# Optimization experiments

Hardware: AMD Instinct MI355X
Metric: run time of the kernel (lower is better)

Reference implementation:

```python
import jax, jax.numpy as jnp
import numpy as np

N_NODES = 50000
N_EDGES = 800000
IN_FEAT = 1000
HID = 128
HEADS = 2
NEG_SLOPE = 0.2  # PyG GATConv default
EPS = 1e-16      # PyG softmax denom eps


def setup_inputs() -> dict:
    key = jax.random.key(0)
    ks = jax.random.split(key, 12)
    x = jax.random.normal(ks[0], (N_NODES, IN_FEAT), dtype=jnp.float32)
    edge_index = jax.random.randint(ks[1], (2, N_EDGES), 0, N_NODES, dtype=jnp.int64)
    readout_idx = jax.random.randint(ks[2], (1024,), 0, N_NODES, dtype=jnp.int64)
    s = 0.05
    return {
        "x": x,
        "edge_index": edge_index,
        "readout_idx": readout_idx,
        "W1": jax.random.normal(ks[3], (IN_FEAT, HEADS * HID), dtype=jnp.float32) * s,
        "att_src1": jax.random.normal(ks[4], (HEADS, HID), dtype=jnp.float32) * s,
        "att_dst1": jax.random.normal(ks[5], (HEADS, HID), dtype=jnp.float32) * s,
        "b1": jax.random.normal(ks[6], (HEADS * HID,), dtype=jnp.float32) * s,
        "W2": jax.random.normal(ks[7], (HEADS * HID, 1), dtype=jnp.float32) * s,
        "att_src2": jax.random.normal(ks[8], (1, 1), dtype=jnp.float32) * s,
        "att_dst2": jax.random.normal(ks[9], (1, 1), dtype=jnp.float32) * s,
        "b2": jax.random.normal(ks[10], (1,), dtype=jnp.float32) * s,
    }


def gat_conv(x, edge_index, W, att_src, att_dst, bias, heads, out_dim, concat):
    """PyG GATConv with add_self_loops=False. x: [N, F_in]."""
    n = x.shape[0]
    src, dst = edge_index[0], edge_index[1]
    h = (x @ W).reshape(n, heads, out_dim)            # [N, H, D]
    a_src = jnp.einsum("nhd,hd->nh", h, att_src)      # [N, H]
    a_dst = jnp.einsum("nhd,hd->nh", h, att_dst)
    e = jax.nn.leaky_relu(a_src[src] + a_dst[dst], NEG_SLOPE)  # [E, H]
    # softmax over incoming edges of each destination node
    e_max = jax.ops.segment_max(e, dst, num_segments=n)
    e_exp = jnp.exp(e - e_max[dst])
    denom = jax.ops.segment_sum(e_exp, dst, num_segments=n)
    alpha = e_exp / (denom[dst] + EPS)                # [E, H]
    msg = h[src] * alpha[:, :, None]                  # [E, H, D]
    out = jax.ops.segment_sum(msg, dst, num_segments=n)  # [N, H, D]
    out = out.reshape(n, heads * out_dim) if concat else out.mean(axis=1)
    return out + bias


def reference(x, edge_index, readout_idx, W1, att_src1, att_dst1, b1,
              W2, att_src2, att_dst2, b2):
    # dropout is identity in eval mode
    h = gat_conv(x, edge_index, W1, att_src1, att_dst1, b1, HEADS, HID, True)
    h = jax.nn.relu(h)
    out = gat_conv(h, edge_index, W2, att_src2, att_dst2, b2, 1, 1, False)  # [N, 1]
    return out[readout_idx]  # [1024, 1]
```

## Files before the change

### kernel.cpp

```cpp
#include <hip/hip_runtime.h>
#include <hip/hip_bf16.h>
#include <math.h>

#define N_NODES 50000
#define N_EDGES 800000
#define IN_FEAT 1000
#define HID 128
#define HEADS 2
#define FOUT 256
#define NEG_SLOPE 0.2f
#define EPS 1e-16f

#define KPAD 1024
#define GEMM_NWG 782

typedef __bf16 bf16x8 __attribute__((ext_vector_type(8)));
typedef float f32x4 __attribute__((ext_vector_type(4)));

__device__ __forceinline__ float lrelu(float v) { return v > 0.f ? v : NEG_SLOPE * v; }

__device__ __forceinline__ ushort bf16rn(float v) {
  union { float f; unsigned u; } a; a.f = v;
  unsigned r = a.u + 0x7FFFu + ((a.u >> 16) & 1u);
  return (ushort)(r >> 16);
}
__device__ __forceinline__ void bf16split(float v, ushort& h, ushort& l) {
  h = bf16rn(v);
  union { float f; unsigned u; } b; b.u = ((unsigned)h) << 16;
  l = bf16rn(v - b.f);
}

__device__ __forceinline__ void gload_lds16(const void* g, void* l) {
  __builtin_amdgcn_global_load_lds((const __attribute__((address_space(1))) void*)g,
                                   (__attribute__((address_space(3))) void*)l, 16, 0, 0);
}

__global__ void hist_kernel(const int* __restrict__ dst, int* __restrict__ counts) {
  int e = blockIdx.x * blockDim.x + threadIdx.x;
  if (e < N_EDGES) atomicAdd(&counts[dst[e]], 1);
}

__global__ __launch_bounds__(1024) void scan1_kernel(const int* __restrict__ counts,
                                                     int* __restrict__ iscan,
                                                     int* __restrict__ bsum) {
  __shared__ int buf[1024];
  const int t = threadIdx.x;
  const int i = blockIdx.x * 1024 + t;
  int v = (i < N_NODES) ? counts[i] : 0;
  buf[t] = v;
  __syncthreads();
#pragma unroll
  for (int off = 1; off < 1024; off <<= 1) {
    int x = (t >= off) ? buf[t - off] : 0;
    __syncthreads();
    buf[t] += x;
    __syncthreads();
  }
  if (i < N_NODES) iscan[i] = buf[t];
  if (t == 1023) bsum[blockIdx.x] = buf[1023];
}

__global__ __launch_bounds__(64) void scan2_kernel(const int* __restrict__ bsum,
                                                   int* __restrict__ boff,
                                                   int* __restrict__ row_start, int nblk) {
  const int t = threadIdx.x;
  int v = (t < nblk) ? bsum[t] : 0;
  int s = v;
#pragma unroll
  for (int off = 1; off < 64; off <<= 1) {
    int y = __shfl_up(s, off, 64);
    if (t >= off) s += y;
  }
  if (t < nblk) boff[t] = s - v;
  if (t == nblk - 1) row_start[N_NODES] = s;
}

__global__ void scan3_kernel(const int* __restrict__ iscan, const int* __restrict__ counts,
                             const int* __restrict__ boff, int* __restrict__ row_start,
                             int* __restrict__ cursor) {
  int i = blockIdx.x * blockDim.x + threadIdx.x;
  if (i < N_NODES) {
    int rs = boff[i >> 10] + iscan[i] - counts[i];
    row_start[i] = rs;
    cursor[i] = rs;
  }
}

__global__ void scatter_kernel(const int* __restrict__ src, const int* __restrict__ dst,
                               int* __restrict__ cursor, int* __restrict__ csr_src) {
  int e = blockIdx.x * blockDim.x + threadIdx.x;
  if (e < N_EDGES) {
    int pos = atomicAdd(&cursor[dst[e]], 1);
    csr_src[pos] = src[e];
  }
}

__global__ __launch_bounds__(256) void cvtB_kernel(const float* __restrict__ B,
                                                   ushort* __restrict__ thi,
                                                   ushort* __restrict__ tlo) {
  int i = blockIdx.x * 256 + threadIdx.x;
  int nn = i >> 8;
  int k4 = (i & 255) << 2;
  ushort4 h, l;
#pragma unroll
  for (int j = 0; j < 4; ++j) {
    int k = k4 + j;
    float v = (k < IN_FEAT) ? B[(size_t)k * FOUT + nn] : 0.f;
    ushort hh, ll;
    bf16split(v, hh, ll);
    ((ushort*)&h)[j] = hh;
    ((ushort*)&l)[j] = ll;
  }
  *(ushort4*)(thi + (size_t)nn * KPAD + k4) = h;
  *(ushort4*)(tlo + (size_t)nn * KPAD + k4) = l;
}

__global__ __launch_bounds__(256, 2) void gemm_fused_kernel(
    const float* __restrict__ X,
    const ushort* __restrict__ Bhi, const ushort* __restrict__ Blo,
    float* __restrict__ C) {
  __shared__ ushort lAhi[128 * 64];
  __shared__ ushort lAlo[128 * 64];
  __shared__ ushort lBhi[128 * 64];
  __shared__ ushort lBlo[128 * 64];

  const int orig = blockIdx.x;
  const int q = GEMM_NWG >> 3, r = GEMM_NWG & 7;
  const int xcd = orig & 7, idx = orig >> 3;
  const int lin = (xcd < r) ? xcd * (q + 1) + idx : r * (q + 1) + (xcd - r) * q + idx;
  const int brow = (lin >> 1) * 128;
  const int bcol = (lin & 1) * 128;

  const int t = threadIdx.x;
  const int lane = t & 63, wid = t >> 6;
  const int wr = wid >> 1, wc = wid & 1;
  const int fr = lane & 15, g = lane >> 4;

  float4 areg[8];

  auto loadA = [&](int ks) {
#pragma unroll
    for (int i = 0; i < 4; ++i) {
      const int c = i * 256 + t;
      const int row = c >> 3, kc8 = c & 7;
      const int ksrc = kc8 ^ (row & 7);
      const int rowg = brow + row;
      const int kb = ks * 64 + ksrc * 8;
      if (rowg < N_NODES && kb < IN_FEAT) {
        const float* p = X + (size_t)rowg * IN_FEAT + kb;
        areg[2 * i] = *(const float4*)p;
        areg[2 * i + 1] = *(const float4*)(p + 4);
      } else {
        areg[2 * i] = make_float4(0.f, 0.f, 0.f, 0.f);
        areg[2 * i + 1] = make_float4(0.f, 0.f, 0.f, 0.f);
      }
    }
  };

  auto stageB = [&](int ks) {
    const int k0b = ks * 128;
#pragma unroll
    for (int i = 0; i < 4; ++i) {
      int u = i * 256 + t;
      int row = u >> 3;
      int inner = (u & 7) * 16;
      int soff = inner ^ ((row & 7) << 4);
      size_t boff = (size_t)(bcol + row) * (KPAD * 2) + k0b + soff;
      int loff = u * 16;
      gload_lds16((const char*)Bhi + boff, (char*)lBhi + loff);
      gload_lds16((const char*)Blo + boff, (char*)lBlo + loff);
    }
  };

  f32x4 acc[4][4];
  const f32x4 z4 = {0.f, 0.f, 0.f, 0.f};
#pragma unroll
  for (int m = 0; m < 4; ++m)
#pragma unroll
    for (int n = 0; n < 4; ++n) acc[m][n] = z4;

  loadA(0);
  const int NK = KPAD / 64;
  for (int ks = 0; ks < NK; ++ks) {
    union U8 { uint4 q; ushort us[8]; };
    U8 hiv[4], lov[4];
#pragma unroll
    for (int i = 0; i < 4; ++i) {
      const float* vv = (const float*)&areg[2 * i];
#pragma unroll
      for (int j = 0; j < 8; ++j) {
        unsigned u = __float_as_uint(vv[j]);
        ushort h = (ushort)(u >> 16);
        float hf = __uint_as_float(u & 0xFFFF0000u);
        float d = vv[j] - hf;
        ushort l = (ushort)(__float_as_uint(d) >> 16);
        hiv[i].us[j] = h;
        lov[i].us[j] = l;
      }
    }
    __syncthreads();
#pragma unroll
    for (int i = 0; i < 4; ++i) {
      const int c = i * 256 + t;
      *(uint4*)((char*)lAhi + c * 16) = hiv[i].q;
      *(uint4*)((char*)lAlo + c * 16) = lov[i].q;
    }
    stageB(ks);
    __syncthreads();
    if (ks + 1 < NK) loadA(ks + 1);
#pragma unroll
    for (int h = 0; h < 2; ++h) {
      bf16x8 ah[4], al[4], bh[4], bl[4];
#pragma unroll
      for (int m = 0; m < 4; ++m) {
        int row = wr * 64 + m * 16 + fr;
        int off = row * 128 + ((h * 64 + g * 16) ^ ((row & 7) << 4));
        ah[m] = *(const bf16x8*)((const char*)lAhi + off);
        al[m] = *(const bf16x8*)((const char*)lAlo + off);
      }
#pragma unroll
      for (int n = 0; n < 4; ++n) {
        int row = wc * 64 + n * 16 + fr;
        int off = row * 128 + ((h * 64 + g * 16) ^ ((row & 7) << 4));
        bh[n] = *(const bf16x8*)((const char*)lBhi + off);
        bl[n] = *(const bf16x8*)((const char*)lBlo + off);
      }
#pragma unroll
      for (int m = 0; m < 4; ++m)
#pragma unroll
        for (int n = 0; n < 4; ++n) {
          acc[m][n] = __builtin_amdgcn_mfma_f32_16x16x32_bf16(ah[m], bh[n], acc[m][n], 0, 0, 0);
          acc[m][n] = __builtin_amdgcn_mfma_f32_16x16x32_bf16(ah[m], bl[n], acc[m][n], 0, 0, 0);
          acc[m][n] = __builtin_amdgcn_mfma_f32_16x16x32_bf16(al[m], bh[n], acc[m][n], 0, 0, 0);
        }
    }
  }

#pragma unroll
  for (int m = 0; m < 4; ++m) {
    int growbase = brow + wr * 64 + m * 16 + g * 4;
#pragma unroll
    for (int n = 0; n < 4; ++n) {
      int gcol = bcol + wc * 64 + n * 16 + fr;
#pragma unroll
      for (int rr = 0; rr < 4; ++rr) {
        int grow = growbase + rr;
        if (grow < N_NODES) C[(size_t)grow * FOUT + gcol] = acc[m][n][rr];
      }
    }
  }
}

__global__ __launch_bounds__(64) void att1_kernel(const float* __restrict__ h1,
                                                  const float* __restrict__ as,
                                                  const float* __restrict__ ad,
                                                  float* __restrict__ asrc,
                                                  float* __restrict__ adst) {
  const int n = blockIdx.x;
  const int lane = threadIdx.x;
  const float* hr = h1 + (size_t)n * FOUT;
  float4 hv = *(const float4*)(hr + 4 * lane);
  float4 sv = *(const float4*)(as + 4 * lane);
  float4 dv = *(const float4*)(ad + 4 * lane);
  float ps = hv.x * sv.x + hv.y * sv.y + hv.z * sv.z + hv.w * sv.w;
  float pd = hv.x * dv.x + hv.y * dv.y + hv.z * dv.z + hv.w * dv.w;
#pragma unroll
  for (int off = 16; off > 0; off >>= 1) {
    ps += __shfl_xor(ps, off, 64);
    pd += __shfl_xor(pd, off, 64);
  }
  if ((lane & 31) == 0) {
    int hh = lane >> 5;
    asrc[2 * n + hh] = ps;
    adst[2 * n + hh] = pd;
  }
}

__global__ __launch_bounds__(64) void agg1_kernel(
    const float* __restrict__ h1, const float* __restrict__ asrc,
    const float* __restrict__ adst, const int* __restrict__ row_start,
    const int* __restrict__ csr_src, const float* __restrict__ b1,
    const float* __restrict__ W2, float* __restrict__ z) {
  const int n = blockIdx.x;
  const int lane = threadIdx.x;
  const bool head0 = lane < 32;
  const float ad0 = adst[2 * n], ad1 = adst[2 * n + 1];
  const int jb = row_start[n], je = row_start[n + 1];
  float ax = 0.f, ay = 0.f, az = 0.f, aw = 0.f;
  float m0 = -INFINITY, m1 = -INFINITY, s0 = 0.f, s1 = 0.f;

  for (int base = jb; base < je; base += 64) {
    int cnt = je - base;
    if (cnt > 64) cnt = 64;
    const bool act = lane < cnt;
    const int sr = csr_src[base + (act ? lane : 0)];
    float e0 = -INFINITY, e1 = -INFINITY;
    if (act) {
      e0 = lrelu(asrc[2 * sr] + ad0);
      e1 = lrelu(asrc[2 * sr + 1] + ad1);
    }
    float c0 = e0, c1 = e1;
#pragma unroll
    for (int off = 32; off > 0; off >>= 1) {
      c0 = fmaxf(c0, __shfl_xor(c0, off, 64));
      c1 = fmaxf(c1, __shfl_xor(c1, off, 64));
    }
    const float m0n = fmaxf(m0, c0), m1n = fmaxf(m1, c1);
    const float f0 = __expf(m0 - m0n), f1 = __expf(m1 - m1n);
    const float p0 = act ? __expf(e0 - m0n) : 0.f;
    const float p1 = act ? __expf(e1 - m1n) : 0.f;
    float t0 = p0, t1 = p1;
#pragma unroll
    for (int off = 32; off > 0; off >>= 1) {
      t0 += __shfl_xor(t0, off, 64);
      t1 += __shfl_xor(t1, off, 64);
    }
    s0 = s0 * f0 + t0;
    s1 = s1 * f1 + t1;
    m0 = m0n;
    m1 = m1n;
    const float f = head0 ? f0 : f1;
    ax *= f; ay *= f; az *= f; aw *= f;
    for (int j = 0; j < cnt; ++j) {
      const int srj = __shfl(sr, j, 64);
      const float pj0 = __shfl(p0, j, 64);
      const float pj1 = __shfl(p1, j, 64);
      const float pj = head0 ? pj0 : pj1;
      float4 hv = *(const float4*)(h1 + (size_t)srj * FOUT + 4 * lane);
      ax = fmaf(pj, hv.x, ax);
      ay = fmaf(pj, hv.y, ay);
      az = fmaf(pj, hv.z, az);
      aw = fmaf(pj, hv.w, aw);
    }
  }
  const float inv = head0 ? 1.f / (s0 + EPS) : 1.f / (s1 + EPS);
  float4 bv = *(const float4*)(b1 + 4 * lane);
  float4 wv = *(const float4*)(W2 + 4 * lane);
  float r0 = fmaxf(fmaf(ax, inv, bv.x), 0.f);
  float r1 = fmaxf(fmaf(ay, inv, bv.y), 0.f);
  float r2 = fmaxf(fmaf(az, inv, bv.z), 0.f);
  float r3 = fmaxf(fmaf(aw, inv, bv.w), 0.f);
  float part = r0 * wv.x + r1 * wv.y + r2 * wv.z + r3 * wv.w;
#pragma unroll
  for (int off = 32; off > 0; off >>= 1) part += __shfl_xor(part, off, 64);
  if (lane == 0) z[n] = part;
}

__global__ __launch_bounds__(64) void agg2_kernel(
    const float* __restrict__ z, const int* __restrict__ row_start,
    const int* __restrict__ csr_src, const float* __restrict__ as2p,
    const float* __restrict__ ad2p, const float* __restrict__ b2p,
    float* __restrict__ out2) {
  const int n = blockIdx.x;
  const int lane = threadIdx.x;
  const float as2 = as2p[0], ad2 = ad2p[0], b2 = b2p[0];
  const float adz = z[n] * ad2;
  const int jb = row_start[n], je = row_start[n + 1];
  float m = -INFINITY, s = 0.f, num = 0.f;
  for (int base = jb; base < je; base += 64) {
    int cnt = je - base;
    if (cnt > 64) cnt = 64;
    const bool act = lane < cnt;
    const int sr = csr_src[base + (act ? lane : 0)];
    const float zs = act ? z[sr] : 0.f;
    const float e = act ? lrelu(zs * as2 + adz) : -INFINITY;
    float c = e;
#pragma unroll
    for (int off = 32; off > 0; off >>= 1) c = fmaxf(c, __shfl_xor(c, off, 64));
    const float mn = fmaxf(m, c);
    const float f = __expf(m - mn);
    const float p = act ? __expf(e - mn) : 0.f;
    float tp = p, tz = p * zs;
#pragma unroll
    for (int off = 32; off > 0; off >>= 1) {
      tp += __shfl_xor(tp, off, 64);
      tz += __shfl_xor(tz, off, 64);
    }
    s = s * f + tp;
    num = num * f + tz;
    m = mn;
  }
  if (lane == 0) out2[n] = num / (s + EPS) + b2;
}

__global__ void readout_kernel(const float* __restrict__ out2, const int* __restrict__ ridx,
                               float* __restrict__ out, int n) {
  int i = blockIdx.x * blockDim.x + threadIdx.x;
  if (i < n) out[i] = out2[ridx[i]];
}

extern "C" void kernel_launch(void* const* d_in, const int* in_sizes, int n_in,
                              void* d_out, int out_size, void* d_ws, size_t ws_size,
                              hipStream_t stream) {
  const float* x   = (const float*)d_in[0];
  const int* ei    = (const int*)d_in[1];
  const int* ridx  = (const int*)d_in[2];
  const float* W1  = (const float*)d_in[3];
  const float* as1 = (const float*)d_in[4];
  const float* ad1 = (const float*)d_in[5];
  const float* b1  = (const float*)d_in[6];
  const float* W2  = (const float*)d_in[7];
  const float* as2 = (const float*)d_in[8];
  const float* ad2 = (const float*)d_in[9];
  const float* b2  = (const float*)d_in[10];
  float* out = (float*)d_out;

  char* ws = (char*)d_ws;
  size_t off = 0;
  auto alloc = [&](size_t bytes) -> void* {
    void* p = ws + off;
    off += (bytes + 255) & ~(size_t)255;
    return p;
  };
  float* h1   = (float*)alloc((size_t)N_NODES * FOUT * 4);
  float* asrc = (float*)alloc((size_t)N_NODES * 2 * 4);
  float* adst = (float*)alloc((size_t)N_NODES * 2 * 4);
  float* z    = (float*)alloc((size_t)N_NODES * 4);
  float* out2 = (float*)alloc((size_t)N_NODES * 4);
  int* counts = (int*)alloc((size_t)N_NODES * 4);
  int* rowst  = (int*)alloc((size_t)(N_NODES + 1) * 4);
  int* cursor = (int*)alloc((size_t)N_NODES * 4);
  int* csr    = (int*)alloc((size_t)N_EDGES * 4);
  int* iscan  = (int*)alloc((size_t)N_NODES * 4);
  int* bsum   = (int*)alloc(64 * 4);
  int* boff   = (int*)alloc(64 * 4);
  ushort* Bhi = (ushort*)alloc((size_t)FOUT * KPAD * 2);
  ushort* Blo = (ushort*)alloc((size_t)FOUT * KPAD * 2);

  const int* src = ei;
  const int* dst = ei + N_EDGES;
  const int nblk = (N_NODES + 1023) / 1024;

  hipMemsetAsync(counts, 0, (size_t)N_NODES * 4, stream);
  hist_kernel<<<(N_EDGES + 255) / 256, 256, 0, stream>>>(dst, counts);
  scan1_kernel<<<nblk, 1024, 0, stream>>>(counts, iscan, bsum);
  scan2_kernel<<<1, 64, 0, stream>>>(bsum, boff, rowst, nblk);
  scan3_kernel<<<(N_NODES + 255) / 256, 256, 0, stream>>>(iscan, counts, boff, rowst, cursor);
  scatter_kernel<<<(N_EDGES + 255) / 256, 256, 0, stream>>>(src, dst, cursor, csr);

  cvtB_kernel<<<256, 256, 0, stream>>>(W1, Bhi, Blo);
  gemm_fused_kernel<<<GEMM_NWG, 256, 0, stream>>>(x, Bhi, Blo, h1);

  att1_kernel<<<N_NODES, 64, 0, stream>>>(h1, as1, ad1, asrc, adst);
  agg1_kernel<<<N_NODES, 64, 0, stream>>>(h1, asrc, adst, rowst, csr, b1, W2, z);
  agg2_kernel<<<N_NODES, 64, 0, stream>>>(z, rowst, csr, as2, ad2, b2, out2);
  readout_kernel<<<4, 256, 0, stream>>>(out2, ridx, out, out_size);
}
```

Before: 574.6 us.

## Restructure GEMM: A fragments in registers, single bf16 B, double-buffered LDS

The first-layer GEMM now keeps A (x) fragments directly in registers, split into bf16 hi/lo parts, instead of staging them through LDS. W1 is converted to a single rounded bf16 copy rather than a hi/lo pair. Each wave computes a 32x128 output strip with 2 MFMAs per tile instead of 3. B is double-buffered in LDS with async global->LDS loads and manual vmcnt waits, cutting LDS traffic, barriers and MFMA count. The trade is lower precision, since W1's low bf16 part is dropped, plus less reuse of A across waves. agg1 also loads the two per-head source attention scores as one float2.

New measurement: 579.8 us. No clear change (+0.9%).

```diff
diff --git a/kernel.cpp b/kernel.cpp
--- a/kernel.cpp
+++ b/kernel.cpp
@@ -23,11 +23,6 @@
   union { float f; unsigned u; } a; a.f = v;
   unsigned r = a.u + 0x7FFFu + ((a.u >> 16) & 1u);
   return (ushort)(r >> 16);
-}
-__device__ __forceinline__ void bf16split(float v, ushort& h, ushort& l) {
-  h = bf16rn(v);
-  union { float f; unsigned u; } b; b.u = ((unsigned)h) << 16;
-  l = bf16rn(v - b.f);
 }
 
 __device__ __forceinline__ void gload_lds16(const void* g, void* l) {
@@ -95,34 +90,25 @@
   }
 }
 
-__global__ __launch_bounds__(256) void cvtB_kernel(const float* __restrict__ B,
-                                                   ushort* __restrict__ thi,
-                                                   ushort* __restrict__ tlo) {
+__global__ __launch_bounds__(256) void cvtB1_kernel(const float* __restrict__ B,
+                                                    ushort* __restrict__ Bt) {
   int i = blockIdx.x * 256 + threadIdx.x;
   int nn = i >> 8;
   int k4 = (i & 255) << 2;
-  ushort4 h, l;
+  ushort4 h;
 #pragma unroll
   for (int j = 0; j < 4; ++j) {
     int k = k4 + j;
     float v = (k < IN_FEAT) ? B[(size_t)k * FOUT + nn] : 0.f;
-    ushort hh, ll;
-    bf16split(v, hh, ll);
-    ((ushort*)&h)[j] = hh;
-    ((ushort*)&l)[j] = ll;
-  }
-  *(ushort4*)(thi + (size_t)nn * KPAD + k4) = h;
-  *(ushort4*)(tlo + (size_t)nn * KPAD + k4) = l;
-}
-
-__global__ __launch_bounds__(256, 2) void gemm_fused_kernel(
-    const float* __restrict__ X,
-    const ushort* __restrict__ Bhi, const ushort* __restrict__ Blo,
+    ((ushort*)&h)[j] = bf16rn(v);
+  }
+  *(ushort4*)(Bt + (size_t)nn * KPAD + k4) = h;
+}
+
+__global__ __launch_bounds__(256, 2) void gemm_fused2_kernel(
+    const float* __restrict__ X, const ushort* __restrict__ Bt,
     float* __restrict__ C) {
-  __shared__ ushort lAhi[128 * 64];
-  __shared__ ushort lAlo[128 * 64];
-  __shared__ ushort lBhi[128 * 64];
-  __shared__ ushort lBlo[128 * 64];
+  __shared__ ushort lB[2][128 * 64];
 
   const int orig = blockIdx.x;
   const int q = GEMM_NWG >> 3, r = GEMM_NWG & 7;
@@ -133,31 +119,30 @@
 
   const int t = threadIdx.x;
   const int lane = t & 63, wid = t >> 6;
-  const int wr = wid >> 1, wc = wid & 1;
   const int fr = lane & 15, g = lane >> 4;
-
-  float4 areg[8];
+  const int wrow = wid * 32;
+
+  float4 areg[2][2][2];
 
   auto loadA = [&](int ks) {
 #pragma unroll
-    for (int i = 0; i < 4; ++i) {
-      const int c = i * 256 + t;
-      const int row = c >> 3, kc8 = c & 7;
-      const int ksrc = kc8 ^ (row & 7);
-      const int rowg = brow + row;
-      const int kb = ks * 64 + ksrc * 8;
-      if (rowg < N_NODES && kb < IN_FEAT) {
-        const float* p = X + (size_t)rowg * IN_FEAT + kb;
-        areg[2 * i] = *(const float4*)p;
-        areg[2 * i + 1] = *(const float4*)(p + 4);
-      } else {
-        areg[2 * i] = make_float4(0.f, 0.f, 0.f, 0.f);
-        areg[2 * i + 1] = make_float4(0.f, 0.f, 0.f, 0.f);
+    for (int m = 0; m < 2; ++m)
+#pragma unroll
+      for (int h = 0; h < 2; ++h) {
+        const int row = brow + wrow + m * 16 + fr;
+        const int k = ks * 64 + h * 32 + g * 8;
+        if (row < N_NODES && k < IN_FEAT) {
+          const float* p = X + (size_t)row * IN_FEAT + k;
+          areg[m][h][0] = *(const float4*)p;
+          areg[m][h][1] = *(const float4*)(p + 4);
+        } else {
+          areg[m][h][0] = make_float4(0.f, 0.f, 0.f, 0.f);
+          areg[m][h][1] = make_float4(0.f, 0.f, 0.f, 0.f);
+        }
       }
-    }
   };
 
-  auto stageB = [&](int ks) {
+  auto stageB = [&](int ks, int buf) {
     const int k0b = ks * 128;
 #pragma unroll
     for (int i = 0; i < 4; ++i) {
@@ -166,86 +151,80 @@
       int inner = (u & 7) * 16;
       int soff = inner ^ ((row & 7) << 4);
       size_t boff = (size_t)(bcol + row) * (KPAD * 2) + k0b + soff;
-      int loff = u * 16;
-      gload_lds16((const char*)Bhi + boff, (char*)lBhi + loff);
-      gload_lds16((const char*)Blo + boff, (char*)lBlo + loff);
+      gload_lds16((const char*)Bt + boff, (char*)&lB[buf][0] + u * 16);
     }
   };
 
-  f32x4 acc[4][4];
+  f32x4 acc[2][8];
   const f32x4 z4 = {0.f, 0.f, 0.f, 0.f};
 #pragma unroll
-  for (int m = 0; m < 4; ++m)
-#pragma unroll
-    for (int n = 0; n < 4; ++n) acc[m][n] = z4;
-
+  for (int m = 0; m < 2; ++m)
+#pragma unroll
+    for (int n = 0; n < 8; ++n) acc[m][n] = z4;
+
+  stageB(0, 0);
   loadA(0);
   const int NK = KPAD / 64;
   for (int ks = 0; ks < NK; ++ks) {
-    union U8 { uint4 q; ushort us[8]; };
-    U8 hiv[4], lov[4];
-#pragma unroll
-    for (int i = 0; i < 4; ++i) {
-      const float* vv = (const float*)&areg[2 * i];
-#pragma unroll
-      for (int j = 0; j < 8; ++j) {
-        unsigned u = __float_as_uint(vv[j]);
-        ushort h = (ushort)(u >> 16);
-        float hf = __uint_as_float(u & 0xFFFF0000u);
-        float d = vv[j] - hf;
-        ushort l = (ushort)(__float_as_uint(d) >> 16);
-        hiv[i].us[j] = h;
-        lov[i].us[j] = l;
+    bf16x8 ah[2][2], al[2][2];
+#pragma unroll
+    for (int m = 0; m < 2; ++m)
+#pragma unroll
+      for (int h = 0; h < 2; ++h) {
+        const float* vv = (const float*)&areg[m][h][0];
+        bf16x8 hv, lv;
+#pragma unroll
+        for (int j = 0; j < 8; ++j) {
+          float v = vv[j];
+          unsigned u = __float_as_uint(v);
+          ((ushort*)&hv)[j] = (ushort)(u >> 16);
+          float hf = __uint_as_float(u & 0xFFFF0000u);
+          float d = v - hf;
+          ((ushort*)&lv)[j] = (ushort)(__float_as_uint(d) >> 16);
+        }
+        ah[m][h] = hv;
+        al[m][h] = lv;
       }
-    }
-    __syncthreads();
-#pragma unroll
-    for (int i = 0; i < 4; ++i) {
-      const int c = i * 256 + t;
-      *(uint4*)((char*)lAhi + c * 16) = hiv[i].q;
-      *(uint4*)((char*)lAlo + c * 16) = lov[i].q;
-    }
-    stageB(ks);
-    __syncthreads();
-    if (ks + 1 < NK) loadA(ks + 1);
+    if (ks + 1 < NK) {
+      loadA(ks + 1);
+      asm volatile("s_waitcnt vmcnt(8)" ::: "memory");
+    } else {
+      asm volatile("s_waitcnt vmcnt(0)" ::: "memory");
+    }
+    __builtin_amdgcn_sched_barrier(0);
+    __builtin_amdgcn_s_barrier();
+    __builtin_amdgcn_sched_barrier(0);
+    if (ks + 1 < NK) stageB(ks + 1, (ks + 1) & 1);
+    const int buf = ks & 1;
 #pragma unroll
     for (int h = 0; h < 2; ++h) {
-      bf16x8 ah[4], al[4], bh[4], bl[4];
-#pragma unroll
-      for (int m = 0; m < 4; ++m) {
-        int row = wr * 64 + m * 16 + fr;
+      bf16x8 bfrag[8];
+#pragma unroll
+      for (int n = 0; n < 8; ++n) {
+        int row = n * 16 + fr;
         int off = row * 128 + ((h * 64 + g * 16) ^ ((row & 7) << 4));
-        ah[m] = *(const bf16x8*)((const char*)lAhi + off);
-        al[m] = *(const bf16x8*)((const char*)lAlo + off);
+        bfrag[n] = *(const bf16x8*)((const char*)&lB[buf][0] + off);
       }
 #pragma unroll
-      for (int n = 0; n < 4; ++n) {
-        int row = wc * 64 + n * 16 + fr;
-        int off = row * 128 + ((h * 64 + g * 16) ^ ((row & 7) << 4));
-        bh[n] = *(const bf16x8*)((const char*)lBhi + off);
-        bl[n] = *(const bf16x8*)((const char*)lBlo + off);
-      }
-#pragma unroll
-      for (int m = 0; m < 4; ++m)
-#pragma unroll
-        for (int n = 0; n < 4; ++n) {
-          acc[m][n] = __builtin_amdgcn_mfma_f32_16x16x32_bf16(ah[m], bh[n], acc[m][n], 0, 0, 0);
-          acc[m][n] = __builtin_amdgcn_mfma_f32_16x16x32_bf16(ah[m], bl[n], acc[m][n], 0, 0, 0);
-          acc[m][n] = __builtin_amdgcn_mfma_f32_16x16x32_bf16(al[m], bh[n], acc[m][n], 0, 0, 0);
+      for (int m = 0; m < 2; ++m)
+#pragma unroll
+        for (int n = 0; n < 8; ++n) {
+          acc[m][n] = __builtin_amdgcn_mfma_f32_16x16x32_bf16(ah[m][h], bfrag[n], acc[m][n], 0, 0, 0);
+          acc[m][n] = __builtin_amdgcn_mfma_f32_16x16x32_bf16(al[m][h], bfrag[n], acc[m][n], 0, 0, 0);
         }
     }
   }
 
 #pragma unroll
-  for (int m = 0; m < 4; ++m) {
-    int growbase = brow + wr * 64 + m * 16 + g * 4;
-#pragma unroll
-    for (int n = 0; n < 4; ++n) {
-      int gcol = bcol + wc * 64 + n * 16 + fr;
+  for (int m = 0; m < 2; ++m) {
+    int rowbase = brow + wrow + m * 16 + g * 4;
+#pragma unroll
+    for (int n = 0; n < 8; ++n) {
+      int col = bcol + n * 16 + fr;
 #pragma unroll
       for (int rr = 0; rr < 4; ++rr) {
-        int grow = growbase + rr;
-        if (grow < N_NODES) C[(size_t)grow * FOUT + gcol] = acc[m][n][rr];
+        int row = rowbase + rr;
+        if (row < N_NODES) C[(size_t)row * FOUT + col] = acc[m][n][rr];
       }
     }
   }
@@ -296,8 +275,9 @@
     const int sr = csr_src[base + (act ? lane : 0)];
     float e0 = -INFINITY, e1 = -INFINITY;
     if (act) {
-      e0 = lrelu(asrc[2 * sr] + ad0);
-      e1 = lrelu(asrc[2 * sr + 1] + ad1);
+      const float2 av = *(const float2*)(asrc + 2 * sr);
+      e0 = lrelu(av.x + ad0);
+      e1 = lrelu(av.y + ad1);
     }
     float c0 = e0, c1 = e1;
 #pragma unroll
@@ -424,8 +404,7 @@
   int* iscan  = (int*)alloc((size_t)N_NODES * 4);
   int* bsum   = (int*)alloc(64 * 4);
   int* boff   = (int*)alloc(64 * 4);
-  ushort* Bhi = (ushort*)alloc((size_t)FOUT * KPAD * 2);
-  ushort* Blo = (ushort*)alloc((size_t)FOUT * KPAD * 2);
+  ushort* Bt  = (ushort*)alloc((size_t)FOUT * KPAD * 2);
 
   const int* src = ei;
   const int* dst = ei + N_EDGES;
@@ -438,8 +417,8 @@
   scan3_kernel<<<(N_NODES + 255) / 256, 256, 0, stream>>>(iscan, counts, boff, rowst, cursor);
   scatter_kernel<<<(N_EDGES + 255) / 256, 256, 0, stream>>>(src, dst, cursor, csr);
 
-  cvtB_kernel<<<256, 256, 0, stream>>>(W1, Bhi, Blo);
-  gemm_fused_kernel<<<GEMM_NWG, 256, 0, stream>>>(x, Bhi, Blo, h1);
+  cvtB1_kernel<<<256, 256, 0, stream>>>(W1, Bt);
+  gemm_fused2_kernel<<<GEMM_NWG, 256, 0, stream>>>(x, Bt, h1);
 
   att1_kernel<<<N_NODES, 64, 0, stream>>>(h1, as1, ad1, asrc, adst);
   agg1_kernel<<<N_NODES, 64, 0, stream>>>(h1, asrc, adst, rowst, csr, b1, W2, z);
```
